# Optimization experiments

Hardware: AMD Instinct MI355X
Metric: run time of the kernel (lower is better)

## Reference

```python
import jax, jax.numpy as jnp
import numpy as np

N = 8_000_000   # total nodes across the batch
B = 2048        # number of graphs (segments)
L1 = 1.0 / 50.0


def _bce(p, t):
    # elementwise BCE matching torch.nn.BCELoss: logs clamped at -100
    logp = jnp.clip(jnp.log(p), -100.0)
    log1mp = jnp.clip(jnp.log1p(-p), -100.0)
    return -(t * logp + (1.0 - t) * log1mp)


def setup_inputs() -> dict:
    key = jax.random.key(0)
    k1, k2, k3, k4, k5, k6 = jax.random.split(key, 6)
    y_mus_pred = jax.random.uniform(k1, (N,), dtype=jnp.float32)
    y_mus = jax.random.uniform(k2, (N,), dtype=jnp.float32)
    y_sat_pred = jax.random.uniform(k3, (B,), dtype=jnp.float32)
    y_sat = jax.random.uniform(k4, (B,), dtype=jnp.float32)
    batch = jnp.sort(jax.random.randint(k5, (N,), 0, B, dtype=jnp.int32))
    mask = jax.random.randint(k6, (N,), 0, 2, dtype=jnp.int32)
    return {"y_mus_pred": y_mus_pred, "y_mus": y_mus,
            "y_sat_pred": y_sat_pred, "y_sat": y_sat,
            "batch": batch, "mask": mask}


def reference(y_mus_pred, y_mus, y_sat_pred, y_sat, batch, mask):
    m = mask.astype(y_mus_pred.dtype)
    # per-node BCE on masked predictions (torch: bce_mus(pred*mask, target), reduction='sum' per graph)
    bce = _bce(y_mus_pred * m, y_mus)                      # [N]
    seg_bce = jax.ops.segment_sum(bce, batch, num_segments=B)  # [B]
    seg_cnt = jax.ops.segment_sum(m, batch, num_segments=B)    # [B] = sum(mask) per graph
    per_graph = jnp.where(seg_cnt > 0, seg_bce / jnp.maximum(seg_cnt, 1.0), 0.0)
    total = per_graph.sum()
    # scalar saturation BCE (mean reduction) scaled by L1
    total = total + _bce(y_sat_pred, y_sat).mean() * jnp.asarray(L1, y_sat_pred.dtype)
    return total
```

## Files before the change

### kernel.cpp

```cpp
#include <hip/hip_runtime.h>

#define BLOCK 256
#define NB    2048
#define CHUNK 1024

typedef float fx4 __attribute__((ext_vector_type(4)));
typedef int   ix4 __attribute__((ext_vector_type(4)));

__device__ __forceinline__ float bce_elem(float p, float t) {
    float lp  = fmaxf(__logf(p), -100.0f);
    float l1p = fmaxf(__logf(1.0f - p), -100.0f);
    return -__builtin_fmaf(t, lp - l1p, l1p);
}

__device__ __forceinline__ int wave_lower_bound(const int* __restrict__ a, int n, int v) {
    const int lane = threadIdx.x & 63;
    int lo = 0, hi = n;
    while (hi - lo > 64) {
        int range  = hi - lo;
        int stride = range / 65 + 1;
        int idx    = lo + (lane + 1) * stride;
        bool lt    = (idx < hi) && (a[idx] < v);
        int  c     = __popcll(__ballot(lt));
        int  nlo   = lo + c * stride;
        int  nhi   = nlo + stride;
        if (nhi > hi) nhi = hi;
        lo = nlo; hi = nhi;
    }
    int idx = lo + lane;
    bool ge = (idx >= hi) || (a[idx] >= v);
    unsigned long long bal = __ballot(ge);
    return bal ? (lo + __ffsll(bal) - 1) : hi;
}

__global__ __launch_bounds__(256) void bounds_kernel(
    const int* __restrict__ batch, int* __restrict__ st, int n, int Bseg)
{
    const int W = blockIdx.x * 4 + (threadIdx.x >> 6);
    if (W <= Bseg) {
        int r = wave_lower_bound(batch, n, W);
        if ((threadIdx.x & 63) == 0) st[W] = r;
    }
}

__device__ __forceinline__ int seg_of_tab(const int* __restrict__ st,
                                          int Bseg, int n, int e) {
    int s = (int)(((long long)e * (long long)Bseg) / (long long)n);
    if (s > Bseg - 1) s = Bseg - 1;
    while (st[s] > e) --s;
    while (st[s + 1] <= e) ++s;
    return s;
}

__global__ __launch_bounds__(BLOCK, 8) void stream_kernel(
    const float* __restrict__ pred, const float* __restrict__ tgt,
    const int* __restrict__ mask, const int* __restrict__ st,
    int* __restrict__ eseg, float* __restrict__ eb, float* __restrict__ ec,
    float* __restrict__ gb, float* __restrict__ gc,
    int n, int Bseg, int nchunks)
{
    const int tid = threadIdx.x;
    const int wid = tid >> 6;

    __shared__ int   sh_s0, sh_sL, sh_bnd, sh_simple;
    __shared__ float red[BLOCK / 64][4];

    for (int c = blockIdx.x; c < nchunks; c += NB) {
        const int base = c << 10;
        const int last = min(base + CHUNK - 1, n - 1);

        if (tid == 0) {
            const int s0 = seg_of_tab(st, Bseg, n, base);
            const int sL = seg_of_tab(st, Bseg, n, last);
            sh_s0  = s0;
            sh_sL  = sL;
            sh_bnd = st[sL];
            sh_simple = (st[s0 + 1] >= st[sL]) ? 1 : 0;
        }
        __syncthreads();
        const int s0 = sh_s0, sL = sh_sL, bnd = sh_bnd, simple = sh_simple;

        float a0b = 0.f, a0c = 0.f, a1b = 0.f, a1c = 0.f;
        const int e0 = base + (tid << 2);

        if (simple) {
            if (e0 + 3 < n) {
                fx4 p = __builtin_nontemporal_load(
                            reinterpret_cast<const fx4*>(pred) + (e0 >> 2));
                fx4 t = __builtin_nontemporal_load(
                            reinterpret_cast<const fx4*>(tgt)  + (e0 >> 2));
                ix4 m = __builtin_nontemporal_load(
                            reinterpret_cast<const ix4*>(mask) + (e0 >> 2));
                #pragma unroll
                for (int j = 0; j < 4; ++j) {
                    float mf = (float)m[j];
                    float v  = bce_elem(p[j] * mf, t[j]);
                    if (e0 + j < bnd) { a0b += v; a0c += mf; }
                    else              { a1b += v; a1c += mf; }
                }
            } else if (e0 < n) {
                for (int j = 0; j < 4 && e0 + j < n; ++j) {
                    const int e  = e0 + j;
                    float mf = (float)mask[e];
                    float v  = bce_elem(pred[e] * mf, tgt[e]);
                    if (e < bnd) { a0b += v; a0c += mf; }
                    else         { a1b += v; a1c += mf; }
                }
            }
        } else {
            for (int j = 0; j < 4; ++j) {
                const int e = e0 + j;
                if (e < n) {
                    float mf = (float)mask[e];
                    float v  = bce_elem(pred[e] * mf, tgt[e]);
                    const int s = seg_of_tab(st, Bseg, n, e);
                    atomicAdd(&gb[s], v);
                    atomicAdd(&gc[s], mf);
                }
            }
        }

        #pragma unroll
        for (int o = 32; o > 0; o >>= 1) {
            a0b += __shfl_xor(a0b, o);  a0c += __shfl_xor(a0c, o);
            a1b += __shfl_xor(a1b, o);  a1c += __shfl_xor(a1c, o);
        }
        if ((tid & 63) == 0) {
            red[wid][0] = a0b;  red[wid][1] = a0c;
            red[wid][2] = a1b;  red[wid][3] = a1c;
        }
        __syncthreads();
        if (tid == 0) {
            float sb0 = 0, sc0 = 0, sb1 = 0, sc1 = 0;
            #pragma unroll
            for (int w = 0; w < BLOCK / 64; ++w) {
                sb0 += red[w][0];  sc0 += red[w][1];
                sb1 += red[w][2];  sc1 += red[w][3];
            }
            eseg[2 * c]     = s0;  eb[2 * c]     = sb0;  ec[2 * c]     = sc0;
            eseg[2 * c + 1] = sL;  eb[2 * c + 1] = sb1;  ec[2 * c + 1] = sc1;
        }
        __syncthreads();
    }
}

__global__ __launch_bounds__(256) void pergraph_kernel(
    const int* __restrict__ st, const int* __restrict__ eseg,
    const float* __restrict__ eb, const float* __restrict__ ec,
    const float* __restrict__ gb, const float* __restrict__ gc,
    const float* __restrict__ sat_pred, const float* __restrict__ sat_tgt,
    float* __restrict__ out, int Bseg)
{
    const int tid  = threadIdx.x;
    const int wid  = tid >> 6;
    const int lane = tid & 63;
    const int S    = blockIdx.x * 4 + wid;

    float pg = 0.f;
    if (S < Bseg) {
        float sb = 0.f, sc = 0.f;
        const int ss = st[S], se = st[S + 1];
        if (ss < se) {
            const int ilo = 2 * (ss >> 10);
            const int ihi = 2 * ((se - 1) >> 10) + 1;
            for (int i = ilo + lane; i <= ihi; i += 64) {
                if (eseg[i] == S) { sb += eb[i]; sc += ec[i]; }
            }
        }
        if (lane == 0) { sb += gb[S]; sc += gc[S]; }
        #pragma unroll
        for (int o = 32; o > 0; o >>= 1) {
            sb += __shfl_xor(sb, o);  sc += __shfl_xor(sc, o);
        }
        if (lane == 0) {
            pg = (sc > 0.f) ? sb / fmaxf(sc, 1.f) : 0.f;
            pg += bce_elem(sat_pred[S], sat_tgt[S]) * ((1.0f / 50.0f) / (float)Bseg);
        }
    }
    __shared__ float ws[4];
    if (lane == 0) ws[wid] = pg;
    __syncthreads();
    if (tid == 0) atomicAdd(out, (ws[0] + ws[1]) + (ws[2] + ws[3]));
}

extern "C" void kernel_launch(void* const* d_in, const int* in_sizes, int n_in,
                              void* d_out, int out_size, void* d_ws, size_t ws_size,
                              hipStream_t stream) {
    const float* y_mus_pred = (const float*)d_in[0];
    const float* y_mus      = (const float*)d_in[1];
    const float* y_sat_pred = (const float*)d_in[2];
    const float* y_sat      = (const float*)d_in[3];
    const int*   batch      = (const int*)d_in[4];
    const int*   mask       = (const int*)d_in[5];

    const int n    = in_sizes[0];
    const int Bseg = in_sizes[2];

    const int nchunks = (n + CHUNK - 1) / CHUNK;

    int*   st   = (int*)d_ws;
    int*   eseg = st + (Bseg + 1);
    float* eb   = (float*)(eseg + 2 * nchunks);
    float* ec   = eb + 2 * nchunks;
    float* gb   = ec + 2 * nchunks;
    float* gc   = gb + Bseg;

    hipMemsetAsync(gb, 0, 2 * Bseg * sizeof(float), stream);
    hipMemsetAsync(d_out, 0, sizeof(float), stream);

    bounds_kernel<<<(Bseg + 4) / 4, 256, 0, stream>>>(batch, st, n, Bseg);
    stream_kernel<<<NB, BLOCK, 0, stream>>>(
        y_mus_pred, y_mus, mask, st, eseg, eb, ec, gb, gc, n, Bseg, nchunks);
    pergraph_kernel<<<(Bseg + 3) / 4, 256, 0, stream>>>(
        st, eseg, eb, ec, gb, gc, y_sat_pred, y_sat, (float*)d_out, Bseg);
}
```

Baseline: 162.7 us.

## Drop segment-bounds kernel; find chunk boundaries directly from batch ids

Removes the bounds_kernel that binary-searched segment starts and the gb/gc global atomic accumulators and their memset. Each chunk now reads its first and last batch ids and binary-searches the boundary inside the chunk. The rare multi-segment chunks are handled serially by one thread, which adds whole interior segments straight into the output. Vector loads are issued before the block barrier, and the per-graph kernel locates its entries by a wave-wide lower_bound over eseg. This cuts one launch and the bounds preprocessing, at the cost of a slow serial path when a chunk spans more than two segments.

```diff
diff --git a/kernel.cpp b/kernel.cpp
--- a/kernel.cpp
+++ b/kernel.cpp
@@ -33,31 +33,11 @@
     return bal ? (lo + __ffsll(bal) - 1) : hi;
 }
 
-__global__ __launch_bounds__(256) void bounds_kernel(
-    const int* __restrict__ batch, int* __restrict__ st, int n, int Bseg)
-{
-    const int W = blockIdx.x * 4 + (threadIdx.x >> 6);
-    if (W <= Bseg) {
-        int r = wave_lower_bound(batch, n, W);
-        if ((threadIdx.x & 63) == 0) st[W] = r;
-    }
-}
-
-__device__ __forceinline__ int seg_of_tab(const int* __restrict__ st,
-                                          int Bseg, int n, int e) {
-    int s = (int)(((long long)e * (long long)Bseg) / (long long)n);
-    if (s > Bseg - 1) s = Bseg - 1;
-    while (st[s] > e) --s;
-    while (st[s + 1] <= e) ++s;
-    return s;
-}
-
 __global__ __launch_bounds__(BLOCK, 8) void stream_kernel(
     const float* __restrict__ pred, const float* __restrict__ tgt,
-    const int* __restrict__ mask, const int* __restrict__ st,
+    const int* __restrict__ batch, const int* __restrict__ mask,
     int* __restrict__ eseg, float* __restrict__ eb, float* __restrict__ ec,
-    float* __restrict__ gb, float* __restrict__ gc,
-    int n, int Bseg, int nchunks)
+    float* __restrict__ out, int n, int nchunks)
 {
     const int tid = threadIdx.x;
     const int wid = tid >> 6;
@@ -68,29 +48,42 @@
     for (int c = blockIdx.x; c < nchunks; c += NB) {
         const int base = c << 10;
         const int last = min(base + CHUNK - 1, n - 1);
+        const int e0   = base + (tid << 2);
+        const bool full = (e0 + 3 < n);
+
+        fx4 p = {0.f, 0.f, 0.f, 0.f};
+        fx4 t = {0.f, 0.f, 0.f, 0.f};
+        ix4 m = {0, 0, 0, 0};
+        if (full) {
+            p = __builtin_nontemporal_load(
+                    reinterpret_cast<const fx4*>(pred) + (e0 >> 2));
+            t = __builtin_nontemporal_load(
+                    reinterpret_cast<const fx4*>(tgt)  + (e0 >> 2));
+            m = __builtin_nontemporal_load(
+                    reinterpret_cast<const ix4*>(mask) + (e0 >> 2));
+        }
 
         if (tid == 0) {
-            const int s0 = seg_of_tab(st, Bseg, n, base);
-            const int sL = seg_of_tab(st, Bseg, n, last);
-            sh_s0  = s0;
-            sh_sL  = sL;
-            sh_bnd = st[sL];
-            sh_simple = (st[s0 + 1] >= st[sL]) ? 1 : 0;
+            const int s0 = batch[base];
+            const int sL = batch[last];
+            int bnd = base;
+            if (sL != s0) {
+                int lo = base + 1, hi = last;
+                while (lo < hi) {
+                    int mid = (lo + hi) >> 1;
+                    if (batch[mid] < sL) lo = mid + 1; else hi = mid;
+                }
+                bnd = lo;
+            }
+            sh_s0 = s0;  sh_sL = sL;  sh_bnd = bnd;
+            sh_simple = (sL <= s0 + 1) ? 1 : 0;
         }
         __syncthreads();
         const int s0 = sh_s0, sL = sh_sL, bnd = sh_bnd, simple = sh_simple;
 
         float a0b = 0.f, a0c = 0.f, a1b = 0.f, a1c = 0.f;
-        const int e0 = base + (tid << 2);
-
         if (simple) {
-            if (e0 + 3 < n) {
-                fx4 p = __builtin_nontemporal_load(
-                            reinterpret_cast<const fx4*>(pred) + (e0 >> 2));
-                fx4 t = __builtin_nontemporal_load(
-                            reinterpret_cast<const fx4*>(tgt)  + (e0 >> 2));
-                ix4 m = __builtin_nontemporal_load(
-                            reinterpret_cast<const ix4*>(mask) + (e0 >> 2));
+            if (full) {
                 #pragma unroll
                 for (int j = 0; j < 4; ++j) {
                     float mf = (float)m[j];
@@ -107,17 +100,6 @@
                     else         { a1b += v; a1c += mf; }
                 }
             }
-        } else {
-            for (int j = 0; j < 4; ++j) {
-                const int e = e0 + j;
-                if (e < n) {
-                    float mf = (float)mask[e];
-                    float v  = bce_elem(pred[e] * mf, tgt[e]);
-                    const int s = seg_of_tab(st, Bseg, n, e);
-                    atomicAdd(&gb[s], v);
-                    atomicAdd(&gc[s], mf);
-                }
-            }
         }
 
         #pragma unroll
@@ -131,25 +113,46 @@
         }
         __syncthreads();
         if (tid == 0) {
-            float sb0 = 0, sc0 = 0, sb1 = 0, sc1 = 0;
-            #pragma unroll
-            for (int w = 0; w < BLOCK / 64; ++w) {
-                sb0 += red[w][0];  sc0 += red[w][1];
-                sb1 += red[w][2];  sc1 += red[w][3];
+            if (simple) {
+                float sb0 = 0, sc0 = 0, sb1 = 0, sc1 = 0;
+                #pragma unroll
+                for (int w = 0; w < BLOCK / 64; ++w) {
+                    sb0 += red[w][0];  sc0 += red[w][1];
+                    sb1 += red[w][2];  sc1 += red[w][3];
+                }
+                eseg[2 * c]     = s0;  eb[2 * c]     = sb0;  ec[2 * c]     = sc0;
+                eseg[2 * c + 1] = sL;  eb[2 * c + 1] = sb1;  ec[2 * c + 1] = sc1;
+            } else {
+                float sb0 = 0, sc0 = 0, sb1 = 0, sc1 = 0;
+                float mb = 0, mc = 0;  int cur = -1;
+                for (int e = base; e <= last; ++e) {
+                    float mf = (float)mask[e];
+                    float v  = bce_elem(pred[e] * mf, tgt[e]);
+                    int   s  = batch[e];
+                    if (s == s0)      { sb0 += v; sc0 += mf; }
+                    else if (s == sL) { sb1 += v; sc1 += mf; }
+                    else {
+                        if (s != cur) {
+                            if (cur >= 0 && mc > 0.f) atomicAdd(out, mb / fmaxf(mc, 1.f));
+                            cur = s;  mb = 0.f;  mc = 0.f;
+                        }
+                        mb += v;  mc += mf;
+                    }
+                }
+                if (cur >= 0 && mc > 0.f) atomicAdd(out, mb / fmaxf(mc, 1.f));
+                eseg[2 * c]     = s0;  eb[2 * c]     = sb0;  ec[2 * c]     = sc0;
+                eseg[2 * c + 1] = sL;  eb[2 * c + 1] = sb1;  ec[2 * c + 1] = sc1;
             }
-            eseg[2 * c]     = s0;  eb[2 * c]     = sb0;  ec[2 * c]     = sc0;
-            eseg[2 * c + 1] = sL;  eb[2 * c + 1] = sb1;  ec[2 * c + 1] = sc1;
         }
         __syncthreads();
     }
 }
 
 __global__ __launch_bounds__(256) void pergraph_kernel(
-    const int* __restrict__ st, const int* __restrict__ eseg,
-    const float* __restrict__ eb, const float* __restrict__ ec,
-    const float* __restrict__ gb, const float* __restrict__ gc,
+    const int* __restrict__ eseg, const float* __restrict__ eb,
+    const float* __restrict__ ec,
     const float* __restrict__ sat_pred, const float* __restrict__ sat_tgt,
-    float* __restrict__ out, int Bseg)
+    float* __restrict__ out, int nentries, int Bseg)
 {
     const int tid  = threadIdx.x;
     const int wid  = tid >> 6;
@@ -158,16 +161,14 @@
 
     float pg = 0.f;
     if (S < Bseg) {
+        const int idx = wave_lower_bound(eseg, nentries, S);
         float sb = 0.f, sc = 0.f;
-        const int ss = st[S], se = st[S + 1];
-        if (ss < se) {
-            const int ilo = 2 * (ss >> 10);
-            const int ihi = 2 * ((se - 1) >> 10) + 1;
-            for (int i = ilo + lane; i <= ihi; i += 64) {
-                if (eseg[i] == S) { sb += eb[i]; sc += ec[i]; }
-            }
-        }
-        if (lane == 0) { sb += gb[S]; sc += gc[S]; }
+        for (int w = 0;; ++w) {
+            const int i = idx + w * 64 + lane;
+            const bool hit = (i < nentries) && (eseg[i] == S);
+            if (hit) { sb += eb[i]; sc += ec[i]; }
+            if (__popcll(__ballot(hit)) < 64) break;
+        }
         #pragma unroll
         for (int o = 32; o > 0; o >>= 1) {
             sb += __shfl_xor(sb, o);  sc += __shfl_xor(sc, o);
@@ -196,21 +197,16 @@
     const int n    = in_sizes[0];
     const int Bseg = in_sizes[2];
 
-    const int nchunks = (n + CHUNK - 1) / CHUNK;
-
-    int*   st   = (int*)d_ws;
-    int*   eseg = st + (Bseg + 1);
-    float* eb   = (float*)(eseg + 2 * nchunks);
-    float* ec   = eb + 2 * nchunks;
-    float* gb   = ec + 2 * nchunks;
-    float* gc   = gb + Bseg;
-
-    hipMemsetAsync(gb, 0, 2 * Bseg * sizeof(float), stream);
+    const int nchunks  = (n + CHUNK - 1) / CHUNK;
+    const int nentries = 2 * nchunks;
+
+    int*   eseg = (int*)d_ws;
+    float* eb   = (float*)(eseg + nentries);
+    float* ec   = eb + nentries;
+
     hipMemsetAsync(d_out, 0, sizeof(float), stream);
-
-    bounds_kernel<<<(Bseg + 4) / 4, 256, 0, stream>>>(batch, st, n, Bseg);
     stream_kernel<<<NB, BLOCK, 0, stream>>>(
-        y_mus_pred, y_mus, mask, st, eseg, eb, ec, gb, gc, n, Bseg, nchunks);
+        y_mus_pred, y_mus, batch, mask, eseg, eb, ec, (float*)d_out, n, nchunks);
     pergraph_kernel<<<(Bseg + 3) / 4, 256, 0, stream>>>(
-        st, eseg, eb, ec, gb, gc, y_sat_pred, y_sat, (float*)d_out, Bseg);
-}
+        eseg, eb, ec, y_sat_pred, y_sat, (float*)d_out, nentries, Bseg);
+}
```

New measurement: 154.8 us. 4.9% less time.
